# Kernel optimization log

Measured on AMD Instinct MI355X. Metric: run time of the kernel, lower is better.

The kernel has to match this reference:

```python
import jax, jax.numpy as jnp
import numpy as np

B, T, E, UNITS = 64, 256, 1024, 1024

def hard_sigmoid(x):
    # Keras K.hard_sigmoid: clip(0.2*x + 0.5, 0, 1)
    return jnp.clip(0.2 * x + 0.5, 0.0, 1.0)

def setup_inputs() -> dict:
    key = jax.random.key(0)
    ks = jax.random.split(key, 11)
    d = {
        "all_inputs": jax.random.normal(ks[0], (B, T, E + UNITS), dtype=jnp.float32),
        "h0": jnp.zeros((B, UNITS), dtype=jnp.float32),
    }
    names = ["W_r", "U_r", "C_r", "W_z", "U_z", "C_z", "W", "U", "C"]
    shapes = {"W_r": (UNITS, UNITS), "U_r": (UNITS, UNITS), "C_r": (E, UNITS),
              "W_z": (UNITS, UNITS), "U_z": (UNITS, UNITS), "C_z": (E, UNITS),
              "W": (UNITS, UNITS), "U": (UNITS, UNITS), "C": (E, UNITS)}
    for i, n in enumerate(names):
        d[n] = jax.random.uniform(ks[i + 2], shapes[n], dtype=jnp.float32,
                                  minval=-0.05, maxval=0.05)
    return d

def reference(all_inputs, h0, W_r, U_r, C_r, W_z, U_z, C_z, W, U, C):
    enc = C_r.shape[0]  # encoder_size
    xs = jnp.swapaxes(all_inputs, 0, 1)  # [T, B, E+units]

    def step(h, x):
        ctx = x[:, :enc]       # encoder context
        emb = x[:, enc:]       # decoder embedding input
        r = hard_sigmoid(emb @ W_r + h @ U_r + ctx @ C_r)
        z = hard_sigmoid(emb @ W_z + h @ U_z + ctx @ C_z)
        h_cand = jnp.tanh(emb @ W + (h * r) @ U + ctx @ C)
        h_new = (1.0 - z) * h + z * h_cand
        return h_new, h_new

    _, ys = jax.lax.scan(step, h0, xs)  # ys: [T, B, units]
    return jnp.swapaxes(ys, 0, 1)       # [B, T, units]
```

## Files before the change

kernel.cpp:

```cpp
#include <hip/hip_runtime.h>
#include <hip/hip_bf16.h>
#include <stdint.h>

#define B_   64
#define T_   256
#define KIN  2048
#define N3   3072
#define M_   16384
#define RBLK 256
#define RTHR 256

typedef __attribute__((ext_vector_type(8))) short short8;
typedef __attribute__((ext_vector_type(4))) float f32x4;
typedef unsigned long long u64;

static __device__ __forceinline__ float bf2f(short s) {
    union { float f; uint32_t u; } c; c.u = ((uint32_t)(uint16_t)s) << 16; return c.f;
}
static __device__ __forceinline__ float u16tof(uint32_t u) {
    union { float f; uint32_t x; } c; c.x = u << 16; return c.f;
}
static __device__ __forceinline__ short f2bf(float f) {
    union { float f; uint32_t u; } c; c.f = f;
    uint32_t u = c.u;
    uint32_t r = (u + 0x7fffu + ((u >> 16) & 1u)) >> 16;
    return (short)(uint16_t)r;
}

#define CLDC(dst, ptr) asm volatile("global_load_dwordx4 %0, %1, off sc0 sc1" : "=v"(dst) : "v"(ptr))
#define CLDU16(dst, ptr) asm volatile("global_load_ushort %0, %1, off"        : "=v"(dst) : "v"(ptr))
static __device__ __forceinline__ void cst8(void* p, u64 v) {
    asm volatile("global_store_dwordx2 %0, %1, off sc0 sc1" :: "v"(p), "v"(v) : "memory");
}

__global__ __launch_bounds__(256)
void k_prep_w(const float* __restrict__ Wr, const float* __restrict__ Ur, const float* __restrict__ Cr,
              const float* __restrict__ Wz, const float* __restrict__ Uz, const float* __restrict__ Cz,
              const float* __restrict__ Wc, const float* __restrict__ Uc, const float* __restrict__ Cc,
              short* __restrict__ WcatT, short* __restrict__ UcatT, short* __restrict__ UcT)
{
    __shared__ float tile[32][33];
    int m = blockIdx.z;
    const float* src; short* dst; int ld, noff, koff;
    switch (m) {
      case 0: src=Cr; dst=WcatT; ld=KIN;  noff=0;    koff=0;    break;
      case 1: src=Wr; dst=WcatT; ld=KIN;  noff=0;    koff=1024; break;
      case 2: src=Cz; dst=WcatT; ld=KIN;  noff=1024; koff=0;    break;
      case 3: src=Wz; dst=WcatT; ld=KIN;  noff=1024; koff=1024; break;
      case 4: src=Cc; dst=WcatT; ld=KIN;  noff=2048; koff=0;    break;
      case 5: src=Wc; dst=WcatT; ld=KIN;  noff=2048; koff=1024; break;
      case 6: src=Ur; dst=UcatT; ld=1024; noff=0;    koff=0;    break;
      case 7: src=Uz; dst=UcatT; ld=1024; noff=1024; koff=0;    break;
      default: src=Uc; dst=UcT;  ld=1024; noff=0;    koff=0;    break;
    }
    int n0 = blockIdx.x * 32, k0 = blockIdx.y * 32;
    int tx = threadIdx.x, ty = threadIdx.y;
    #pragma unroll
    for (int i = 0; i < 32; i += 8)
        tile[ty + i][tx] = src[(long)(k0 + ty + i) * 1024 + (n0 + tx)];
    __syncthreads();
    #pragma unroll
    for (int i = 0; i < 32; i += 8)
        dst[(long)(noff + n0 + ty + i) * ld + koff + k0 + tx] = f2bf(tile[tx][ty + i]);
}

__global__ __launch_bounds__(256)
void k_prep_x(const float* __restrict__ X, short* __restrict__ Xb, long n8)
{
    long i = (long)blockIdx.x * blockDim.x + threadIdx.x;
    long stride = (long)gridDim.x * blockDim.x;
    for (; i < n8; i += stride) {
        const float4* p = (const float4*)(X + i * 8);
        float4 a = p[0], b = p[1];
        short8 o;
        o[0]=f2bf(a.x); o[1]=f2bf(a.y); o[2]=f2bf(a.z); o[3]=f2bf(a.w);
        o[4]=f2bf(b.x); o[5]=f2bf(b.y); o[6]=f2bf(b.z); o[7]=f2bf(b.w);
        *(short8*)(Xb + i * 8) = o;
    }
}

__global__ __launch_bounds__(256)
void k_init_h(const float* __restrict__ h0, float* __restrict__ h,
              short* __restrict__ hbRM, short* __restrict__ hbF,
              uint32_t* __restrict__ flags)
{
    int i = blockIdx.x * 256 + threadIdx.x;
    float v = h0[i];
    h[i] = v;
    short bv = f2bf(v);
    hbRM[i] = bv;
    int b = i >> 10, k = i & 1023;
    int bg = b >> 4, row = b & 15, kk = k >> 5, ksub = (k & 31) >> 3, e = k & 7;
    hbF[bg * 16384 + kk * 512 + row * 32 + ksub * 8 + e] = bv;
    if (i < 8192) flags[i] = 0;
}

__global__ __launch_bounds__(256)
void k_gemm_x(const short* __restrict__ Xb, const short* __restrict__ WcatT, short* __restrict__ P)
{
    __shared__ short As[128 * 64];
    __shared__ short Bs[128 * 64];
    int tid = threadIdx.x;
    int lane = tid & 63, wave = tid >> 6;
    int i0 = blockIdx.y * 128;
    int n0 = blockIdx.x * 128;
    int wrow = (wave >> 1) * 64, wcol = (wave & 1) * 64;
    f32x4 acc[4][4] = {};

    for (int k0 = 0; k0 < KIN; k0 += 64) {
        __syncthreads();
        #pragma unroll
        for (int j = 0; j < 4; j++) {
            int e = (j * 256 + tid) * 8;
            int row = e >> 6, k = e & 63;
            short8 va = *(const short8*)(Xb    + (long)(i0 + row) * KIN + k0 + k);
            short8 vb = *(const short8*)(WcatT + (long)(n0 + row) * KIN + k0 + k);
            int byt = row * 128 + ((k * 2) ^ ((row & 7) << 4));
            *(short8*)((char*)As + byt) = va;
            *(short8*)((char*)Bs + byt) = vb;
        }
        __syncthreads();
        #pragma unroll
        for (int kk = 0; kk < 64; kk += 32) {
            short8 af[4], bfr[4];
            int kel = kk + (lane >> 4) * 8;
            #pragma unroll
            for (int rt = 0; rt < 4; rt++) {
                int row = wrow + rt * 16 + (lane & 15);
                int byt = row * 128 + ((kel * 2) ^ ((row & 7) << 4));
                af[rt] = *(const short8*)((const char*)As + byt);
            }
            #pragma unroll
            for (int ct = 0; ct < 4; ct++) {
                int row = wcol + ct * 16 + (lane & 15);
                int byt = row * 128 + ((kel * 2) ^ ((row & 7) << 4));
                bfr[ct] = *(const short8*)((const char*)Bs + byt);
            }
            #pragma unroll
            for (int rt = 0; rt < 4; rt++)
                #pragma unroll
                for (int ct = 0; ct < 4; ct++)
                    acc[rt][ct] = __builtin_amdgcn_mfma_f32_16x16x32_bf16(af[rt], bfr[ct], acc[rt][ct], 0, 0, 0);
        }
    }
    #pragma unroll
    for (int rt = 0; rt < 4; rt++)
      #pragma unroll
      for (int ct = 0; ct < 4; ct++)
        #pragma unroll
        for (int r = 0; r < 4; r++) {
            int row = i0 + wrow + rt * 16 + (lane >> 4) * 4 + r;
            int prow = ((row & 255) << 6) | (row >> 8);
            int col = n0 + wcol + ct * 16 + (lane & 15);
            P[(long)prow * N3 + col] = f2bf(acc[rt][ct][r]);
        }
}

static __device__ __forceinline__ void gbar64(uint32_t* flags, uint32_t seq, int grpbase)
{
    asm volatile("s_waitcnt vmcnt(0)" ::: "memory");
    __syncthreads();
    if (threadIdx.x == 0)
        __hip_atomic_store(flags + blockIdx.x * 32, seq, __ATOMIC_RELAXED, __HIP_MEMORY_SCOPE_AGENT);
    if (threadIdx.x < 64) {
        int l = threadIdx.x;
        for (;;) {
            uint32_t v = __hip_atomic_load(flags + (grpbase + l) * 32,
                                           __ATOMIC_RELAXED, __HIP_MEMORY_SCOPE_AGENT);
            if (__all((int)(v >= seq))) break;
        }
    }
    __syncthreads();
}

#define SRCB(s) (((s) >> 6) * 1024 + ((s) & 15) * 64 + (((s) >> 4) & 3) * 16)

__global__ __launch_bounds__(RTHR)
void k_recur5(const short* __restrict__ UcatT, const short* __restrict__ UcT,
              const short* __restrict__ P, const float* __restrict__ hG,
              char* __restrict__ hbF, char* __restrict__ rhF,
              uint32_t* __restrict__ flags, float* __restrict__ out)
{
    __shared__ short wbuf[49152];
    __shared__ short stageS[16384];
    __shared__ float h_lds[256];
    __shared__ float z_lds[256];
    __shared__ short tscr[1280];

    const int tid  = threadIdx.x;
    const int lane = tid & 63, w = tid >> 6;
    const int col16 = lane & 15, rquad = (lane >> 4) * 4;
    const int bg = blockIdx.x >> 6;
    const int cg = blockIdx.x & 63;
    const int c0 = cg * 16;
    const int grpbase = bg * 64;

    #pragma unroll 4
    for (int i = 0; i < 24; i++) {
        int c = tid + i * 256;
        int tau = c >> 11, cc = c & 2047;
        int kk = cc >> 6, l = cc & 63;
        const short* srcp;
        if (tau == 0)      srcp = UcatT + (c0 + (l & 15)) * 1024 + kk * 32 + ((l >> 4) & 3) * 8;
        else if (tau == 1) srcp = UcatT + (1024 + c0 + (l & 15)) * 1024 + kk * 32 + ((l >> 4) & 3) * 8;
        else               srcp = UcT   + (c0 + (l & 15)) * 1024 + kk * 32 + ((l >> 4) & 3) * 8;
        *(short8*)((char*)wbuf + c * 16) = *(const short8*)srcp;
    }
    h_lds[tid] = hG[(bg * 16 + (tid >> 4)) * 1024 + c0 + (tid & 15)];
    __syncthreads();

    short* mytscr = tscr + w * 320;
    const char* exA = hbF + bg * 32768;
    const char* exB = rhF + bg * 32768;
    const int kkp = c0 >> 5, halfp = (c0 >> 4) & 1;
    uint32_t seq = 0;
    uint32_t pr[4], pz[4], pc[4];

    for (int t = 0; t < T_; t++) {
        if (t > 0) {
            out[((long)(bg * 16 + (tid >> 4)) * T_ + (t - 1)) * 1024 + c0 + (tid & 15)] = h_lds[tid];
        }
        {
            short8 v0,v1,v2,v3,v4,v5,v6,v7;
            CLDC(v0, exA + SRCB(tid));
            CLDC(v1, exA + SRCB(tid + 256));
            CLDC(v2, exA + SRCB(tid + 512));
            CLDC(v3, exA + SRCB(tid + 768));
            CLDC(v4, exA + SRCB(tid + 1024));
            CLDC(v5, exA + SRCB(tid + 1280));
            CLDC(v6, exA + SRCB(tid + 1536));
            CLDC(v7, exA + SRCB(tid + 1792));
            const char* Pb = (const char*)(P + ((long)t * 64 + bg * 16) * N3 + c0 + col16);
            if (w == 0) {
                #pragma unroll
                for (int r = 0; r < 4; r++)
                    CLDU16(pr[r], Pb + (long)(rquad + r) * N3 * 2);
                #pragma unroll
                for (int r = 0; r < 4; r++)
                    CLDU16(pc[r], Pb + ((long)(rquad + r) * N3 + 2048) * 2);
            } else if (w == 1) {
                #pragma unroll
                for (int r = 0; r < 4; r++)
                    CLDU16(pz[r], Pb + ((long)(rquad + r) * N3 + 1024) * 2);
            }
            asm volatile("s_waitcnt vmcnt(0)" ::: "memory");
            *(short8*)((char*)stageS + (tid         ) * 16) = v0;
            *(short8*)((char*)stageS + (tid +  256) * 16) = v1;
            *(short8*)((char*)stageS + (tid +  512) * 16) = v2;
            *(short8*)((char*)stageS + (tid +  768) * 16) = v3;
            *(short8*)((char*)stageS + (tid + 1024) * 16) = v4;
            *(short8*)((char*)stageS + (tid + 1280) * 16) = v5;
            *(short8*)((char*)stageS + (tid + 1536) * 16) = v6;
            *(short8*)((char*)stageS + (tid + 1792) * 16) = v7;
        }
        __syncthreads();

        if (w < 2) {
            f32x4 e = {}, o = {};
            const char* wb = (const char*)wbuf + w * 32768;
            #pragma unroll
            for (int kk = 0; kk < 32; kk += 2) {
                short8 a0 = *(const short8*)((const char*)stageS + kk * 1024 + lane * 16);
                short8 b0 = *(const short8*)(wb + kk * 1024 + lane * 16);
                e = __builtin_amdgcn_mfma_f32_16x16x32_bf16(a0, b0, e, 0, 0, 0);
                short8 a1 = *(const short8*)((const char*)stageS + (kk + 1) * 1024 + lane * 16);
                short8 b1 = *(const short8*)(wb + (kk + 1) * 1024 + lane * 16);
                o = __builtin_amdgcn_mfma_f32_16x16x32_bf16(a1, b1, o, 0, 0, 0);
            }
            f32x4 acc = e + o;
            if (w == 0) {
                #pragma unroll
                for (int r = 0; r < 4; r++) {
                    float pre = acc[r] + u16tof(pr[r]);
                    float v = fminf(fmaxf(0.2f * pre + 0.5f, 0.f), 1.f);
                    mytscr[(rquad + r) * 20 + col16] = f2bf(v * h_lds[(rquad + r) * 16 + col16]);
                }
                asm volatile("s_waitcnt lgkmcnt(0)" ::: "memory");
                __builtin_amdgcn_sched_barrier(0);
                u64 vv = *(const u64*)((const char*)mytscr + (lane & 15) * 40 + (lane >> 4) * 8);
                cst8(rhF + bg * 32768 + kkp * 1024 + (lane & 15) * 64 + halfp * 32 + (lane >> 4) * 8, vv);
            } else {
                #pragma unroll
                for (int r = 0; r < 4; r++) {
                    float pre = acc[r] + u16tof(pz[r]);
                    z_lds[(rquad + r) * 16 + col16] = fminf(fmaxf(0.2f * pre + 0.5f, 0.f), 1.f);
                }
            }
        }
        gbar64(flags, ++seq, grpbase);

        {
            short8 v0,v1,v2,v3,v4,v5,v6,v7;
            CLDC(v0, exB + SRCB(tid));
            CLDC(v1, exB + SRCB(tid + 256));
            CLDC(v2, exB + SRCB(tid + 512));
            CLDC(v3, exB + SRCB(tid + 768));
            CLDC(v4, exB + SRCB(tid + 1024));
            CLDC(v5, exB + SRCB(tid + 1280));
            CLDC(v6, exB + SRCB(tid + 1536));
            CLDC(v7, exB + SRCB(tid + 1792));
            asm volatile("s_waitcnt vmcnt(0)" ::: "memory");
            *(short8*)((char*)stageS + (tid         ) * 16) = v0;
            *(short8*)((char*)stageS + (tid +  256) * 16) = v1;
            *(short8*)((char*)stageS + (tid +  512) * 16) = v2;
            *(short8*)((char*)stageS + (tid +  768) * 16) = v3;
            *(short8*)((char*)stageS + (tid + 1024) * 16) = v4;
            *(short8*)((char*)stageS + (tid + 1280) * 16) = v5;
            *(short8*)((char*)stageS + (tid + 1536) * 16) = v6;
            *(short8*)((char*)stageS + (tid + 1792) * 16) = v7;
        }
        __syncthreads();

        if (w == 0) {
            f32x4 e = {}, o = {};
            const char* wb = (const char*)wbuf + 65536;
            #pragma unroll
            for (int kk = 0; kk < 32; kk += 2) {
                short8 a0 = *(const short8*)((const char*)stageS + kk * 1024 + lane * 16);
                short8 b0 = *(const short8*)(wb + kk * 1024 + lane * 16);
                e = __builtin_amdgcn_mfma_f32_16x16x32_bf16(a0, b0, e, 0, 0, 0);
                short8 a1 = *(const short8*)((const char*)stageS + (kk + 1) * 1024 + lane * 16);
                short8 b1 = *(const short8*)(wb + (kk + 1) * 1024 + lane * 16);
                o = __builtin_amdgcn_mfma_f32_16x16x32_bf16(a1, b1, o, 0, 0, 0);
            }
            f32x4 acc = e + o;
            #pragma unroll
            for (int r = 0; r < 4; r++) {
                int idx = (rquad + r) * 16 + col16;
                float pre = acc[r] + u16tof(pc[r]);
                float hc = tanhf(pre);
                float z  = z_lds[idx];
                float ho = h_lds[idx];
                float hn = (1.f - z) * ho + z * hc;
                h_lds[idx] = hn;
                mytscr[(rquad + r) * 20 + col16] = f2bf(hn);
            }
            asm volatile("s_waitcnt lgkmcnt(0)" ::: "memory");
            __builtin_amdgcn_sched_barrier(0);
            u64 vv = *(const u64*)((const char*)mytscr + (lane & 15) * 40 + (lane >> 4) * 8);
            cst8(hbF + bg * 32768 + kkp * 1024 + (lane & 15) * 64 + halfp * 32 + (lane >> 4) * 8, vv);
        }
        gbar64(flags, ++seq, grpbase);
    }

    out[((long)(bg * 16 + (tid >> 4)) * T_ + 255) * 1024 + c0 + (tid & 15)] = h_lds[tid];
}

__global__ __launch_bounds__(256)
void k_stepA(const short* __restrict__ hb, const short* __restrict__ UcatT,
             const short* __restrict__ P, const float* __restrict__ h,
             short* __restrict__ rh, float* __restrict__ zbuf, int t)
{
    int lane = threadIdx.x & 63, wave = threadIdx.x >> 6;
    int wid = blockIdx.x * 4 + wave;
    int ct = wid & 127, rt = wid >> 7;
    int r0 = rt * 16, n0 = ct * 16;
    int lrow = lane & 15, lk = (lane >> 4) * 8;
    f32x4 acc = {0.f, 0.f, 0.f, 0.f};
    const short8* Aptr = (const short8*)(hb    + (r0 + lrow) * 1024 + lk);
    const short8* Bptr = (const short8*)(UcatT + (n0 + lrow) * 1024 + lk);
    #pragma unroll 8
    for (int kk = 0; kk < 32; kk++)
        acc = __builtin_amdgcn_mfma_f32_16x16x32_bf16(Aptr[kk * 4], Bptr[kk * 4], acc, 0, 0, 0);

    int col = n0 + (lane & 15);
    int brb = r0 + (lane >> 4) * 4;
    #pragma unroll
    for (int r = 0; r < 4; r++) {
        int b = brb + r;
        float pre = acc[r] + bf2f(P[((long)t * 64 + b) * N3 + col]);
        float v = fminf(fmaxf(0.2f * pre + 0.5f, 0.f), 1.f);
        if (col < 1024)
            rh[b * 1024 + col] = f2bf(v * h[b * 1024 + col]);
        else
            zbuf[b * 1024 + (col - 1024)] = v;
    }
}

__global__ __launch_bounds__(256)
void k_stepB(const short* __restrict__ rh, const short* __restrict__ UcT,
             const short* __restrict__ P, const float* __restrict__ zbuf,
             float* __restrict__ h, short* __restrict__ hb,
             float* __restrict__ out, int t)
{
    int lane = threadIdx.x & 63, wave = threadIdx.x >> 6;
    int wid = blockIdx.x * 4 + wave;
    int ct = wid & 63, rt = wid >> 6;
    int r0 = rt * 16, n0 = ct * 16;
    int lrow = lane & 15, lk = (lane >> 4) * 8;
    f32x4 acc = {0.f, 0.f, 0.f, 0.f};
    const short8* Aptr = (const short8*)(rh  + (r0 + lrow) * 1024 + lk);
    const short8* Bptr = (const short8*)(UcT + (n0 + lrow) * 1024 + lk);
    #pragma unroll 8
    for (int kk = 0; kk < 32; kk++)
        acc = __builtin_amdgcn_mfma_f32_16x16x32_bf16(Aptr[kk * 4], Bptr[kk * 4], acc, 0, 0, 0);

    int col = n0 + (lane & 15);
    int brb = r0 + (lane >> 4) * 4;
    #pragma unroll
    for (int r = 0; r < 4; r++) {
        int b = brb + r;
        float pre = acc[r] + bf2f(P[((long)t * 64 + b) * N3 + 2048 + col]);
        float hc = tanhf(pre);
        float z  = zbuf[b * 1024 + col];
        float ho = h[b * 1024 + col];
        float hn = (1.f - z) * ho + z * hc;
        h[b * 1024 + col]  = hn;
        hb[b * 1024 + col] = f2bf(hn);
        out[((long)b * T_ + t) * 1024 + col] = hn;
    }
}

extern "C" void kernel_launch(void* const* d_in, const int* in_sizes, int n_in,
                              void* d_out, int out_size, void* d_ws, size_t ws_size,
                              hipStream_t stream)
{
    (void)in_sizes; (void)n_in; (void)out_size; (void)ws_size;
    const float* X   = (const float*)d_in[0];
    const float* h0  = (const float*)d_in[1];
    const float* W_r = (const float*)d_in[2];
    const float* U_r = (const float*)d_in[3];
    const float* C_r = (const float*)d_in[4];
    const float* W_z = (const float*)d_in[5];
    const float* U_z = (const float*)d_in[6];
    const float* C_z = (const float*)d_in[7];
    const float* W   = (const float*)d_in[8];
    const float* U   = (const float*)d_in[9];
    const float* C   = (const float*)d_in[10];

    char* ws = (char*)d_ws;
    size_t off = 0;
    short* WcatT = (short*)(ws + off); off += (size_t)N3 * KIN * 2;
    short* UcatT = (short*)(ws + off); off += (size_t)2048 * 1024 * 2;
    short* UcT   = (short*)(ws + off); off += (size_t)1024 * 1024 * 2;
    short* Xb    = (short*)(ws + off); off += (size_t)M_ * KIN * 2;
    short* P     = (short*)(ws + off); off += (size_t)M_ * N3 * 2;
    float* h     = (float*)(ws + off); off += (size_t)B_ * 1024 * 4;
    short* hbRM  = (short*)(ws + off); off += (size_t)B_ * 1024 * 2;
    short* rhRM  = (short*)(ws + off); off += (size_t)B_ * 1024 * 2;
    float* zbuf  = (float*)(ws + off); off += (size_t)B_ * 1024 * 4;
    char*  hbF   = (char*)(ws + off);  off += (size_t)B_ * 1024 * 2;
    char*  rhF   = (char*)(ws + off);  off += (size_t)B_ * 1024 * 2;
    uint32_t* flags = (uint32_t*)(ws + off); off += 32768;

    k_prep_w<<<dim3(32, 32, 9), dim3(32, 8), 0, stream>>>(W_r, U_r, C_r, W_z, U_z, C_z, W, U, C,
                                                          WcatT, UcatT, UcT);
    k_prep_x<<<2048, 256, 0, stream>>>(X, Xb, (long)M_ * KIN / 8);
    k_init_h<<<256, 256, 0, stream>>>(h0, h, hbRM, (short*)hbF, flags);
    k_gemm_x<<<dim3(N3 / 128, M_ / 128), 256, 0, stream>>>(Xb, WcatT, P);

    float* out = (float*)d_out;
    void* args[] = { (void*)&UcatT, (void*)&UcT, (void*)&P, (void*)&h, (void*)&hbF,
                     (void*)&rhF, (void*)&flags, (void*)&out };
    hipError_t e = hipLaunchCooperativeKernel((const void*)k_recur5, dim3(RBLK), dim3(RTHR),
                                              args, 0, stream);
    if (e != hipSuccess) {
        for (int t = 0; t < T_; t++) {
            k_stepA<<<128, 256, 0, stream>>>(hbRM, UcatT, P, h, rhRM, zbuf, t);
            k_stepB<<<64, 256, 0, stream>>>(rhRM, UcT, P, zbuf, h, hbRM, out, t);
        }
    }
}
```

Before: 2.044 ms.

## Split-K recurrent matvec across all waves and overlap z-gate with barrier

Rewrites the persistent recurrent kernel so each of the four waves loads its own K-slice of h/rh straight into registers and runs an eighth of the MFMAs, with partial sums reduced through LDS. This replaces the previous scheme, where all threads staged the full operand into LDS and only one or two waves did the matvec. The group barrier becomes a split signal/wait, and the z-gate matvec now runs between publishing rh and waiting on the other blocks, overlapping compute with the cross-block sync. The next step's P pre-activations are prefetched at the end of each iteration. The cost is extra LDS reductions and block-level syncs, plus subtler memory-ordering assumptions around the flag protocol.

```diff
diff --git a/kernel.cpp b/kernel.cpp
--- a/kernel.cpp
+++ b/kernel.cpp
@@ -156,36 +156,18 @@
         }
 }
 
-static __device__ __forceinline__ void gbar64(uint32_t* flags, uint32_t seq, int grpbase)
-{
-    asm volatile("s_waitcnt vmcnt(0)" ::: "memory");
-    __syncthreads();
-    if (threadIdx.x == 0)
-        __hip_atomic_store(flags + blockIdx.x * 32, seq, __ATOMIC_RELAXED, __HIP_MEMORY_SCOPE_AGENT);
-    if (threadIdx.x < 64) {
-        int l = threadIdx.x;
-        for (;;) {
-            uint32_t v = __hip_atomic_load(flags + (grpbase + l) * 32,
-                                           __ATOMIC_RELAXED, __HIP_MEMORY_SCOPE_AGENT);
-            if (__all((int)(v >= seq))) break;
-        }
-    }
-    __syncthreads();
-}
-
-#define SRCB(s) (((s) >> 6) * 1024 + ((s) & 15) * 64 + (((s) >> 4) & 3) * 16)
-
 __global__ __launch_bounds__(RTHR)
-void k_recur5(const short* __restrict__ UcatT, const short* __restrict__ UcT,
+void k_recur6(const short* __restrict__ UcatT, const short* __restrict__ UcT,
               const short* __restrict__ P, const float* __restrict__ hG,
               char* __restrict__ hbF, char* __restrict__ rhF,
               uint32_t* __restrict__ flags, float* __restrict__ out)
 {
     __shared__ short wbuf[49152];
-    __shared__ short stageS[16384];
+    __shared__ float pbuf[1024];
+    __shared__ float pbuf2[1024];
     __shared__ float h_lds[256];
     __shared__ float z_lds[256];
-    __shared__ short tscr[1280];
+    __shared__ short tscr[320];
 
     const int tid  = threadIdx.x;
     const int lane = tid & 63, w = tid >> 6;
@@ -209,139 +191,161 @@
     h_lds[tid] = hG[(bg * 16 + (tid >> 4)) * 1024 + c0 + (tid & 15)];
     __syncthreads();
 
-    short* mytscr = tscr + w * 320;
-    const char* exA = hbF + bg * 32768;
-    const char* exB = rhF + bg * 32768;
+    const char* aA  = hbF + bg * 32768 + (w * 8) * 1024 + (lane & 15) * 64 + (lane >> 4) * 16;
+    const char* aB  = rhF + bg * 32768 + (w * 8) * 1024 + (lane & 15) * 64 + (lane >> 4) * 16;
+    const char* wbR = (const char*)wbuf + (w * 8) * 1024 + lane * 16;
+    const char* wbZ = (const char*)wbuf + 32768 + (w * 8) * 1024 + lane * 16;
+    const char* wbC = (const char*)wbuf + 65536 + (w * 8) * 1024 + lane * 16;
     const int kkp = c0 >> 5, halfp = (c0 >> 4) & 1;
-    uint32_t seq = 0;
+    float* mypb  = pbuf  + w * 256 + lane * 4;
+    float* mypb2 = pbuf2 + w * 256 + lane * 4;
+
     uint32_t pr[4], pz[4], pc[4];
+    {
+        const char* Pb = (const char*)(P + (long)(bg * 16) * N3 + c0 + col16);
+        if (w == 0) {
+            #pragma unroll
+            for (int r = 0; r < 4; r++) CLDU16(pr[r], Pb + (long)(rquad + r) * N3 * 2);
+            #pragma unroll
+            for (int r = 0; r < 4; r++) CLDU16(pc[r], Pb + ((long)(rquad + r) * N3 + 2048) * 2);
+        } else if (w == 1) {
+            #pragma unroll
+            for (int r = 0; r < 4; r++) CLDU16(pz[r], Pb + ((long)(rquad + r) * N3 + 1024) * 2);
+        }
+    }
 
     for (int t = 0; t < T_; t++) {
-        if (t > 0) {
+        if (w == 0) {
+            uint32_t tgt = 2u * t;
+            for (;;) {
+                uint32_t v = __hip_atomic_load(flags + (grpbase + lane) * 32,
+                                               __ATOMIC_RELAXED, __HIP_MEMORY_SCOPE_AGENT);
+                if (__all((int)(v >= tgt))) break;
+            }
+        }
+        __syncthreads();
+
+        if (t > 0)
             out[((long)(bg * 16 + (tid >> 4)) * T_ + (t - 1)) * 1024 + c0 + (tid & 15)] = h_lds[tid];
-        }
-        {
-            short8 v0,v1,v2,v3,v4,v5,v6,v7;
-            CLDC(v0, exA + SRCB(tid));
-            CLDC(v1, exA + SRCB(tid + 256));
-            CLDC(v2, exA + SRCB(tid + 512));
-            CLDC(v3, exA + SRCB(tid + 768));
-            CLDC(v4, exA + SRCB(tid + 1024));
-            CLDC(v5, exA + SRCB(tid + 1280));
-            CLDC(v6, exA + SRCB(tid + 1536));
-            CLDC(v7, exA + SRCB(tid + 1792));
-            const char* Pb = (const char*)(P + ((long)t * 64 + bg * 16) * N3 + c0 + col16);
-            if (w == 0) {
-                #pragma unroll
-                for (int r = 0; r < 4; r++)
-                    CLDU16(pr[r], Pb + (long)(rquad + r) * N3 * 2);
-                #pragma unroll
-                for (int r = 0; r < 4; r++)
-                    CLDU16(pc[r], Pb + ((long)(rquad + r) * N3 + 2048) * 2);
-            } else if (w == 1) {
-                #pragma unroll
-                for (int r = 0; r < 4; r++)
-                    CLDU16(pz[r], Pb + ((long)(rquad + r) * N3 + 1024) * 2);
-            }
+
+        short8 a[8];
+        #pragma unroll
+        for (int j = 0; j < 8; j++) CLDC(a[j], aA + j * 1024);
+        asm volatile("s_waitcnt vmcnt(0)" ::: "memory");
+        __builtin_amdgcn_sched_barrier(0);
+
+        f32x4 acc = {};
+        #pragma unroll
+        for (int j = 0; j < 8; j++) {
+            short8 bw = *(const short8*)(wbR + j * 1024);
+            acc = __builtin_amdgcn_mfma_f32_16x16x32_bf16(a[j], bw, acc, 0, 0, 0);
+        }
+        *(f32x4*)mypb = acc;
+        asm volatile("s_waitcnt lgkmcnt(0)" ::: "memory");
+        __syncthreads();
+
+        if (w == 0) {
+            f32x4 s = *(const f32x4*)(pbuf + lane * 4) + *(const f32x4*)(pbuf + 256 + lane * 4)
+                    + *(const f32x4*)(pbuf + 512 + lane * 4) + *(const f32x4*)(pbuf + 768 + lane * 4);
+            #pragma unroll
+            for (int r = 0; r < 4; r++) {
+                float pre = s[r] + u16tof(pr[r]);
+                float v = fminf(fmaxf(0.2f * pre + 0.5f, 0.f), 1.f);
+                tscr[(rquad + r) * 20 + col16] = f2bf(v * h_lds[(rquad + r) * 16 + col16]);
+            }
+            asm volatile("s_waitcnt lgkmcnt(0)" ::: "memory");
+            __builtin_amdgcn_sched_barrier(0);
+            u64 vv = *(const u64*)((const char*)tscr + (lane & 15) * 40 + (lane >> 4) * 8);
+            cst8(rhF + bg * 32768 + kkp * 1024 + (lane & 15) * 64 + halfp * 32 + (lane >> 4) * 8, vv);
             asm volatile("s_waitcnt vmcnt(0)" ::: "memory");
-            *(short8*)((char*)stageS + (tid         ) * 16) = v0;
-            *(short8*)((char*)stageS + (tid +  256) * 16) = v1;
-            *(short8*)((char*)stageS + (tid +  512) * 16) = v2;
-            *(short8*)((char*)stageS + (tid +  768) * 16) = v3;
-            *(short8*)((char*)stageS + (tid + 1024) * 16) = v4;
-            *(short8*)((char*)stageS + (tid + 1280) * 16) = v5;
-            *(short8*)((char*)stageS + (tid + 1536) * 16) = v6;
-            *(short8*)((char*)stageS + (tid + 1792) * 16) = v7;
-        }
-        __syncthreads();
-
-        if (w < 2) {
-            f32x4 e = {}, o = {};
-            const char* wb = (const char*)wbuf + w * 32768;
-            #pragma unroll
-            for (int kk = 0; kk < 32; kk += 2) {
-                short8 a0 = *(const short8*)((const char*)stageS + kk * 1024 + lane * 16);
-                short8 b0 = *(const short8*)(wb + kk * 1024 + lane * 16);
-                e = __builtin_amdgcn_mfma_f32_16x16x32_bf16(a0, b0, e, 0, 0, 0);
-                short8 a1 = *(const short8*)((const char*)stageS + (kk + 1) * 1024 + lane * 16);
-                short8 b1 = *(const short8*)(wb + (kk + 1) * 1024 + lane * 16);
-                o = __builtin_amdgcn_mfma_f32_16x16x32_bf16(a1, b1, o, 0, 0, 0);
-            }
-            f32x4 acc = e + o;
-            if (w == 0) {
-                #pragma unroll
-                for (int r = 0; r < 4; r++) {
-                    float pre = acc[r] + u16tof(pr[r]);
-                    float v = fminf(fmaxf(0.2f * pre + 0.5f, 0.f), 1.f);
-                    mytscr[(rquad + r) * 20 + col16] = f2bf(v * h_lds[(rquad + r) * 16 + col16]);
-                }
-                asm volatile("s_waitcnt lgkmcnt(0)" ::: "memory");
-                __builtin_amdgcn_sched_barrier(0);
-                u64 vv = *(const u64*)((const char*)mytscr + (lane & 15) * 40 + (lane >> 4) * 8);
-                cst8(rhF + bg * 32768 + kkp * 1024 + (lane & 15) * 64 + halfp * 32 + (lane >> 4) * 8, vv);
-            } else {
-                #pragma unroll
-                for (int r = 0; r < 4; r++) {
-                    float pre = acc[r] + u16tof(pz[r]);
-                    z_lds[(rquad + r) * 16 + col16] = fminf(fmaxf(0.2f * pre + 0.5f, 0.f), 1.f);
-                }
-            }
-        }
-        gbar64(flags, ++seq, grpbase);
-
-        {
-            short8 v0,v1,v2,v3,v4,v5,v6,v7;
-            CLDC(v0, exB + SRCB(tid));
-            CLDC(v1, exB + SRCB(tid + 256));
-            CLDC(v2, exB + SRCB(tid + 512));
-            CLDC(v3, exB + SRCB(tid + 768));
-            CLDC(v4, exB + SRCB(tid + 1024));
-            CLDC(v5, exB + SRCB(tid + 1280));
-            CLDC(v6, exB + SRCB(tid + 1536));
-            CLDC(v7, exB + SRCB(tid + 1792));
-            asm volatile("s_waitcnt vmcnt(0)" ::: "memory");
-            *(short8*)((char*)stageS + (tid         ) * 16) = v0;
-            *(short8*)((char*)stageS + (tid +  256) * 16) = v1;
-            *(short8*)((char*)stageS + (tid +  512) * 16) = v2;
-            *(short8*)((char*)stageS + (tid +  768) * 16) = v3;
-            *(short8*)((char*)stageS + (tid + 1024) * 16) = v4;
-            *(short8*)((char*)stageS + (tid + 1280) * 16) = v5;
-            *(short8*)((char*)stageS + (tid + 1536) * 16) = v6;
-            *(short8*)((char*)stageS + (tid + 1792) * 16) = v7;
-        }
-        __syncthreads();
+            if (lane == 0)
+                __hip_atomic_store(flags + blockIdx.x * 32, 2u * t + 1u,
+                                   __ATOMIC_RELAXED, __HIP_MEMORY_SCOPE_AGENT);
+        }
+        f32x4 accz = {};
+        #pragma unroll
+        for (int j = 0; j < 8; j++) {
+            short8 bw = *(const short8*)(wbZ + j * 1024);
+            accz = __builtin_amdgcn_mfma_f32_16x16x32_bf16(a[j], bw, accz, 0, 0, 0);
+        }
+        *(f32x4*)mypb2 = accz;
+        asm volatile("s_waitcnt lgkmcnt(0)" ::: "memory");
 
         if (w == 0) {
-            f32x4 e = {}, o = {};
-            const char* wb = (const char*)wbuf + 65536;
-            #pragma unroll
-            for (int kk = 0; kk < 32; kk += 2) {
-                short8 a0 = *(const short8*)((const char*)stageS + kk * 1024 + lane * 16);
-                short8 b0 = *(const short8*)(wb + kk * 1024 + lane * 16);
-                e = __builtin_amdgcn_mfma_f32_16x16x32_bf16(a0, b0, e, 0, 0, 0);
-                short8 a1 = *(const short8*)((const char*)stageS + (kk + 1) * 1024 + lane * 16);
-                short8 b1 = *(const short8*)(wb + (kk + 1) * 1024 + lane * 16);
-                o = __builtin_amdgcn_mfma_f32_16x16x32_bf16(a1, b1, o, 0, 0, 0);
-            }
-            f32x4 acc = e + o;
+            uint32_t tgt = 2u * t + 1u;
+            for (;;) {
+                uint32_t v = __hip_atomic_load(flags + (grpbase + lane) * 32,
+                                               __ATOMIC_RELAXED, __HIP_MEMORY_SCOPE_AGENT);
+                if (__all((int)(v >= tgt))) break;
+            }
+        }
+        __syncthreads();
+
+        #pragma unroll
+        for (int j = 0; j < 8; j++) CLDC(a[j], aB + j * 1024);
+
+        if (w == 1) {
+            f32x4 sz = *(const f32x4*)(pbuf2 + lane * 4) + *(const f32x4*)(pbuf2 + 256 + lane * 4)
+                     + *(const f32x4*)(pbuf2 + 512 + lane * 4) + *(const f32x4*)(pbuf2 + 768 + lane * 4);
+            #pragma unroll
+            for (int r = 0; r < 4; r++) {
+                float pre = sz[r] + u16tof(pz[r]);
+                z_lds[(rquad + r) * 16 + col16] = fminf(fmaxf(0.2f * pre + 0.5f, 0.f), 1.f);
+            }
+        }
+        asm volatile("s_waitcnt vmcnt(0)" ::: "memory");
+        __builtin_amdgcn_sched_barrier(0);
+
+        f32x4 accc = {};
+        #pragma unroll
+        for (int j = 0; j < 8; j++) {
+            short8 bw = *(const short8*)(wbC + j * 1024);
+            accc = __builtin_amdgcn_mfma_f32_16x16x32_bf16(a[j], bw, accc, 0, 0, 0);
+        }
+        *(f32x4*)mypb = accc;
+        asm volatile("s_waitcnt lgkmcnt(0)" ::: "memory");
+        __syncthreads();
+
+        if (w == 0) {
+            f32x4 s = *(const f32x4*)(pbuf + lane * 4) + *(const f32x4*)(pbuf + 256 + lane * 4)
+                    + *(const f32x4*)(pbuf + 512 + lane * 4) + *(const f32x4*)(pbuf + 768 + lane * 4);
             #pragma unroll
             for (int r = 0; r < 4; r++) {
                 int idx = (rquad + r) * 16 + col16;
-                float pre = acc[r] + u16tof(pc[r]);
+                float pre = s[r] + u16tof(pc[r]);
                 float hc = tanhf(pre);
                 float z  = z_lds[idx];
                 float ho = h_lds[idx];
                 float hn = (1.f - z) * ho + z * hc;
                 h_lds[idx] = hn;
-                mytscr[(rquad + r) * 20 + col16] = f2bf(hn);
+                tscr[(rquad + r) * 20 + col16] = f2bf(hn);
             }
             asm volatile("s_waitcnt lgkmcnt(0)" ::: "memory");
             __builtin_amdgcn_sched_barrier(0);
-            u64 vv = *(const u64*)((const char*)mytscr + (lane & 15) * 40 + (lane >> 4) * 8);
+            u64 vv = *(const u64*)((const char*)tscr + (lane & 15) * 40 + (lane >> 4) * 8);
             cst8(hbF + bg * 32768 + kkp * 1024 + (lane & 15) * 64 + halfp * 32 + (lane >> 4) * 8, vv);
-        }
-        gbar64(flags, ++seq, grpbase);
-    }
+            asm volatile("s_waitcnt vmcnt(0)" ::: "memory");
+            if (lane == 0)
+                __hip_atomic_store(flags + blockIdx.x * 32, 2u * t + 2u,
+                                   __ATOMIC_RELAXED, __HIP_MEMORY_SCOPE_AGENT);
+        }
+
+        {
+            int tn = (t + 1) & 255;
+            const char* Pb = (const char*)(P + ((long)tn * 64 + bg * 16) * N3 + c0 + col16);
+            if (w == 0) {
+                #pragma unroll
+                for (int r = 0; r < 4; r++) CLDU16(pr[r], Pb + (long)(rquad + r) * N3 * 2);
+                #pragma unroll
+                for (int r = 0; r < 4; r++) CLDU16(pc[r], Pb + ((long)(rquad + r) * N3 + 2048) * 2);
+            } else if (w == 1) {
+                #pragma unroll
+                for (int r = 0; r < 4; r++) CLDU16(pz[r], Pb + ((long)(rquad + r) * N3 + 1024) * 2);
+            }
+        }
+    }
+
+    __syncthreads();
 
     out[((long)(bg * 16 + (tid >> 4)) * T_ + 255) * 1024 + c0 + (tid & 15)] = h_lds[tid];
 }
@@ -452,7 +456,7 @@
     float* out = (float*)d_out;
     void* args[] = { (void*)&UcatT, (void*)&UcT, (void*)&P, (void*)&h, (void*)&hbF,
                      (void*)&rhF, (void*)&flags, (void*)&out };
-    hipError_t e = hipLaunchCooperativeKernel((const void*)k_recur5, dim3(RBLK), dim3(RTHR),
+    hipError_t e = hipLaunchCooperativeKernel((const void*)k_recur6, dim3(RBLK), dim3(RTHR),
                                               args, 0, stream);
     if (e != hipSuccess) {
         for (int t = 0; t < T_; t++) {
```

Result: faster. 1.730 ms, median of 2 (-15.4%).
